# Optimization experiments

Hardware: AMD Instinct MI355X
Metric: run time of the kernel (lower is better)

Reference implementation:

```python
import jax, jax.numpy as jnp
import numpy as np

B, T, L = 16, 64, 64
DIN, D, DC, A = 512, 512, 512, 256


def setup_inputs() -> dict:
    key = jax.random.key(0)
    ks = jax.random.split(key, 16)
    g = lambda k, shape, fan: jax.random.normal(k, shape, jnp.float32) / np.float32(np.sqrt(fan))
    return {
        "X": jax.random.normal(ks[0], (B, T, DIN), jnp.float32),
        "context": jax.random.normal(ks[1], (B, L, DC), jnp.float32),
        "parent_t_seq": jax.random.randint(ks[2], (B, T), 0, T),
        "context_mask": jnp.zeros((B, L), jnp.int32),
        "mask": jnp.ones((B, T), jnp.float32),
        # fused gate weights, gate order [i, f, c, o] along last axis
        "Wx": g(ks[3], (DIN, 4 * D), DIN),
        "bx": jnp.zeros((4 * D,), jnp.float32),
        "U": g(ks[4], (D, 4 * D), D),
        "C": g(ks[5], (DC, 4 * D), DC),
        "P": g(ks[6], (D, 4 * D), D),
        "H": g(ks[7], (D, 4 * D), D),
        # context attention
        "att_ctx_W1": g(ks[8], (DC, A), DC),
        "att_b1": jnp.zeros((A,), jnp.float32),
        "att_h_W1": g(ks[9], (D, A), D),
        "att_W2": g(ks[10], (A,), A),
        "att_b2": jnp.zeros((), jnp.float32),
        # history attention
        "hatt_hist_W": g(ks[11], (D, A), D),
        "hatt_hist_b": jnp.zeros((A,), jnp.float32),
        "hatt_h_W1": g(ks[12], (D, A), D),
        "hatt_W2": g(ks[13], (A,), A),
        "hatt_b2": jnp.zeros((), jnp.float32),
    }


def reference(X, context, parent_t_seq, context_mask, mask,
              Wx, bx, U, C, P, H,
              att_ctx_W1, att_b1, att_h_W1, att_W2, att_b2,
              hatt_hist_W, hatt_hist_b, hatt_h_W1, hatt_W2, hatt_b2):
    Bb, Tt, _ = X.shape
    Dd = U.shape[0]
    x4 = X @ Wx + bx                                 # [B,T,4D] precomputed input gates
    ctx_trans = context @ att_ctx_W1 + att_b1        # [B,L,A]
    ts = jnp.arange(Tt)
    batch_idx = jnp.arange(Bb)

    def step(carry, inp):
        h, c, hist = carry                           # h,c [B,D]; hist [B,T,D]
        t, xg, m, par = inp                          # xg [B,4D], m [B], par [B]
        # --- attention over encoder context ---
        ah = jnp.tanh(ctx_trans + (h @ att_h_W1)[:, None, :])   # [B,L,A]
        raw = ah @ att_W2 + att_b2                               # [B,L]
        raw = jnp.where(context_mask > 0, -jnp.inf, raw)
        catt = jax.nn.softmax(raw, axis=-1)
        ctx_vec = jnp.einsum('bl,blc->bc', catt, context)        # [B,DC]
        # --- attention over decoding history (positions < t) ---
        hh = jnp.tanh(hist @ hatt_hist_W + hatt_hist_b + (h @ hatt_h_W1)[:, None, :])  # [B,T,A]
        hraw = hh @ hatt_W2 + hatt_b2                            # [B,T]
        hmask = (ts < t).astype(X.dtype)                         # [T]
        hexp = jnp.exp(hraw - jnp.max(hraw, axis=-1, keepdims=True)) * hmask
        hw = hexp / (jnp.sum(hexp, axis=-1, keepdims=True) + 1e-7)
        h_ctx = jnp.where(t > 0, jnp.einsum('bt,btd->bd', hw, hist), 0.0)
        # --- parent hidden state feed ---
        par_h = jnp.where(t > 0, hist[batch_idx, par], 0.0)      # [B,D]
        # --- fused LSTM gates (tree attention path: U, C, P, H terms) ---
        g = xg + h @ U + ctx_vec @ C + par_h @ P + h_ctx @ H     # [B,4D]
        gi, gf, gc, go = jnp.split(g, 4, axis=-1)
        i = jax.nn.sigmoid(gi)
        f = jax.nn.sigmoid(gf)
        o = jax.nn.sigmoid(go)
        c_new = f * c + i * jnp.tanh(gc)
        h_new = o * jnp.tanh(c_new)
        mm = m[:, None]
        h_new = (1 - mm) * h + mm * h_new
        c_new = (1 - mm) * c + mm * c_new
        hist = jax.lax.dynamic_update_slice(hist, h_new[:, None, :], (0, t, 0))
        return (h_new, c_new, hist), (h_new, c_new, ctx_vec)

    h0 = jnp.zeros((Bb, Dd), X.dtype)
    c0 = jnp.zeros((Bb, Dd), X.dtype)
    hist0 = jnp.zeros((Bb, Tt, Dd), X.dtype)
    xs = (ts, jnp.swapaxes(x4, 0, 1), mask.T, parent_t_seq.T)
    _, (hs, cs, ctxs) = jax.lax.scan(step, (h0, c0, hist0), xs)
    # back to batch-major
    return (jnp.swapaxes(hs, 0, 1), jnp.swapaxes(cs, 0, 1), jnp.swapaxes(ctxs, 0, 1))
```

## Files before the change

kernel.cpp:

```cpp
#include <hip/hip_runtime.h>
#include <cmath>
#include <cstdint>

#define NWG 256
#define NT  256

#define WS_FLAGS 0
#define WS_HC    8192
#define WS_CT    16384
#define WS_CACHE 278528
#define WS_HIST  540672
#define WS_HHP   1064960
#define WS_AHB   1196032

#define OUT_HS  0
#define OUT_CS  524288
#define OUT_CTX 1048576

#define LDS_WT   0
#define LDS_ZS   20544
#define LDS_SCR  28800
#define LDS_GLD  30848
#define LDS_ATT  30976
#define LDS_FLOATS 32448

typedef float vf4 __attribute__((ext_vector_type(4)));
typedef float vf2 __attribute__((ext_vector_type(2)));

struct CAParams {
  const float* X; const float* ctx; const int* parent; const int* cmask; const float* mask;
  const float* Wx; const float* bx; const float* U; const float* C; const float* P; const float* H;
  const float* acW1; const float* ab1; const float* ahW1; const float* aW2; const float* ab2;
  const float* hhW; const float* hhb; const float* hthW1; const float* hW2; const float* hb2;
  float* out; float* ws;
};

__device__ __forceinline__ float tanh_f(float x) {
  x = fminf(15.f, fmaxf(-15.f, x));
  float e = __expf(2.f * x);
  return (e - 1.f) / (e + 1.f);
}
__device__ __forceinline__ float sigm_f(float x) { return 1.f / (1.f + __expf(-x)); }
__device__ __forceinline__ float wsum(float v) {
  #pragma unroll
  for (int m = 32; m; m >>= 1) v += __shfl_xor(v, m, 64);
  return v;
}
__device__ __forceinline__ float wmax(float v) {
  #pragma unroll
  for (int m = 32; m; m >>= 1) v = fmaxf(v, __shfl_xor(v, m, 64));
  return v;
}
__device__ __forceinline__ float hsum32(float v) {
  #pragma unroll
  for (int m = 16; m; m >>= 1) v += __shfl_xor(v, m, 64);
  return v;
}
__device__ __forceinline__ uint32_t f2bf(float f) {
  uint32_t u = __float_as_uint(f);
  return (u + 0x7FFFu + ((u >> 16) & 1u)) >> 16;
}

__device__ __forceinline__ void bst(float* a, float v) {
  asm volatile("global_store_dword %0, %1, off sc0 sc1" :: "v"(a), "v"(v) : "memory");
}
__device__ __forceinline__ void bstu(uint32_t* a, uint32_t v) {
  asm volatile("global_store_dword %0, %1, off sc0 sc1" :: "v"(a), "v"(v) : "memory");
}
__device__ __forceinline__ void bst4(float* a, vf4 v) {
  asm volatile("global_store_dwordx4 %0, %1, off sc0 sc1" :: "v"(a), "v"(v) : "memory");
}
__device__ __forceinline__ void bld8_issue(vf4* r, const float* q0, const float* q1, const float* q2, const float* q3,
                                           const float* q4, const float* q5, const float* q6, const float* q7) {
  asm volatile(
    "global_load_dwordx4 %0, %8, off sc0 sc1\n"
    "global_load_dwordx4 %1, %9, off sc0 sc1\n"
    "global_load_dwordx4 %2, %10, off sc0 sc1\n"
    "global_load_dwordx4 %3, %11, off sc0 sc1\n"
    "global_load_dwordx4 %4, %12, off sc0 sc1\n"
    "global_load_dwordx4 %5, %13, off sc0 sc1\n"
    "global_load_dwordx4 %6, %14, off sc0 sc1\n"
    "global_load_dwordx4 %7, %15, off sc0 sc1"
    : "=&v"(r[0]),"=&v"(r[1]),"=&v"(r[2]),"=&v"(r[3]),"=&v"(r[4]),"=&v"(r[5]),"=&v"(r[6]),"=&v"(r[7])
    : "v"(q0),"v"(q1),"v"(q2),"v"(q3),"v"(q4),"v"(q5),"v"(q6),"v"(q7)
    : "memory");
}
__device__ __forceinline__ void bwait8(vf4* r) {
  asm volatile("s_waitcnt vmcnt(0)"
    : "+v"(r[0]),"+v"(r[1]),"+v"(r[2]),"+v"(r[3]),"+v"(r[4]),"+v"(r[5]),"+v"(r[6]),"+v"(r[7])
    :: "memory");
}

__global__ void __launch_bounds__(NT, 1) condatt_kernel(CAParams p) {
  extern __shared__ float lds[];
  float* wt   = lds + LDS_WT;
  float* zs   = lds + LDS_ZS;
  float* scr  = lds + LDS_SCR;
  float* gld  = lds + LDS_GLD;
  float* aw   = lds + LDS_ATT;
  float* av2  = lds + LDS_ATT + 256;
  float* abv  = lds + LDS_ATT + 512;
  float* araw = lds + LDS_ATT + 768;
  float* asmx = lds + LDS_ATT + 832;
  float* arawZ= lds + LDS_ATT + 896;
  float* hst  = lds + LDS_ATT + 960;

  const int tid = threadIdx.x;
  const int wg  = blockIdx.x;
  float* wsp = p.ws;
  unsigned* flags = (unsigned*)wsp;
  unsigned nbar = 0;

  const int base = 2 * ((wg & 7) * 32 + (wg >> 3));

  __threadfence_system();

  const int kh = tid >> 4, sub = tid & 15, bg = sub >> 2, cp = sub & 3;
  float acc[4][2] = {{0.f,0.f},{0.f,0.f},{0.f,0.f},{0.f,0.f}};
  float hprev = 0.f, cprev = 0.f;

  auto gsync = [&]() {
    asm volatile("s_waitcnt vmcnt(0)" ::: "memory");
    __syncthreads();
    ++nbar;
    if (tid == 0)
      __hip_atomic_store(&flags[wg * 16], nbar, __ATOMIC_RELAXED, __HIP_MEMORY_SCOPE_SYSTEM);
    while (__hip_atomic_load(&flags[tid * 16], __ATOMIC_RELAXED, __HIP_MEMORY_SCOPE_SYSTEM) < nbar)
      __builtin_amdgcn_s_sleep(1);
    __syncthreads();
  };

  {
    for (int j = 0; j < 4; ++j) {
      int rid = wg * 4 + j;
      __syncthreads();
      for (int i = tid; i < 512; i += NT) scr[i] = p.ctx[rid * 512 + i];
      __syncthreads();
      float a0 = 0.f, a1 = 0.f, a2 = 0.f, a3 = 0.f;
      for (int c = 0; c < 512; c += 4) {
        a0 += scr[c+0] * p.acW1[(c+0) * 256 + tid];
        a1 += scr[c+1] * p.acW1[(c+1) * 256 + tid];
        a2 += scr[c+2] * p.acW1[(c+2) * 256 + tid];
        a3 += scr[c+3] * p.acW1[(c+3) * 256 + tid];
      }
      bst(wsp + WS_CT + rid * 256 + tid, p.ab1[tid] + ((a0 + a1) + (a2 + a3)));
    }
    __syncthreads();
    const float* mats[5] = {p.Wx, p.U, p.P, p.C, p.H};
    for (int q = 0; q < 4; ++q) {
      for (int r = tid; r < 2560; r += NT) {
        int m = r >> 9, rr = r & 511;
        vf2 v = *(const vf2*)(mats[m] + rr * 2048 + base + 512 * q);
        *(vf2*)(wt + q * 5136 + r * 2) = v;
      }
    }
    {
      uint32_t* hpd = (uint32_t*)(wsp + WS_HHP);
      for (int i = wg * NT + tid; i < 131072; i += NWG * NT) {
        uint32_t lo = f2bf(p.hthW1[i]);
        uint32_t hi = f2bf(p.hhW[i]);
        bstu(hpd + i, lo | (hi << 16));
      }
      uint32_t* ahd = (uint32_t*)(wsp + WS_AHB);
      for (int j = wg * NT + tid; j < 65536; j += NWG * NT) {
        uint32_t lo = f2bf(p.ahW1[j * 2]);
        uint32_t hi = f2bf(p.ahW1[j * 2 + 1]);
        bstu(ahd + j, lo | (hi << 16));
      }
    }
    if (wg < 16)            { av2[tid] = p.aW2[tid]; }
    else if (wg < 32)       { av2[tid] = p.hW2[tid]; abv[tid] = p.hhb[tid]; }
    #pragma unroll
    for (int j = 0; j < 8; ++j) {
      int i4 = tid + j * NT, b = i4 >> 7, k0 = (i4 << 2) & 511;
      vf4 v = *(const vf4*)(p.X + (b * 64 + 0) * 512 + k0);
      *(vf4*)(zs + b * 516 + k0) = v;
    }
    __syncthreads();
  }

  auto gemm = [&](int comp) {
    const float* wp = wt + cp * 5136 + comp * 1024;
    const float* zb = zs + (bg * 4) * 516;
    #pragma unroll 4
    for (int j = 0; j < 32; ++j) {
      int k = kh + (j << 4);
      vf2 w = *(const vf2*)(wp + k * 2);
      float z0 = zb[k], z1 = zb[516 + k], z2 = zb[1032 + k], z3 = zb[1548 + k];
      acc[0][0] += z0 * w.x; acc[0][1] += z0 * w.y;
      acc[1][0] += z1 * w.x; acc[1][1] += z1 * w.y;
      acc[2][0] += z2 * w.x; acc[2][1] += z2 * w.y;
      acc[3][0] += z3 * w.x; acc[3][1] += z3 * w.y;
    }
  };

  gemm(0);
  gsync();

  for (int t = 0; t < 64; ++t) {
    if (wg < 32) {
      const int b = wg & 15;
      if (tid < 128) {
        vf4 v = {0.f, 0.f, 0.f, 0.f};
        if (t > 0) v = *(const vf4*)(wsp + WS_HIST + (b * 64 + (t - 1)) * 512 + tid * 4);
        *(vf4*)(hst + tid * 4) = v;
      }
      __syncthreads();
      if (wg < 16) {
        const uint16_t* ahb = (const uint16_t*)(wsp + WS_AHB);
        float s = 0.f;
        #pragma unroll 8
        for (int k = 0; k < 512; ++k)
          s += hst[k] * __uint_as_float((uint32_t)ahb[k * 256 + tid] << 16);
        aw[tid] = s;
        __syncthreads();
        {
          int w = tid >> 6, s32 = tid & 31, hi = (tid >> 5) & 1;
          float b2 = *p.ab2;
          for (int l = w * 2 + hi; l < 64; l += 8) {
            float sc = 0.f;
            #pragma unroll
            for (int q = 0; q < 8; ++q) { int a = s32 + (q << 5); sc += av2[a] * tanh_f(wsp[WS_CT + (b * 64 + l) * 256 + a] + aw[a]); }
            sc = hsum32(sc) + b2;
            if (s32 == 0) araw[l] = (p.cmask[b * 64 + l] > 0) ? -INFINITY : sc;
          }
        }
        __syncthreads();
        if (tid < 64) {
          float r = araw[tid];
          float mx = wmax(r);
          float e = __expf(r - mx);
          float sm = wsum(e);
          asmx[tid] = e / sm;
        }
        __syncthreads();
        {
          int db = tid & 127, half = tid >> 7;
          vf4 a0 = {0.f, 0.f, 0.f, 0.f};
          #pragma unroll 4
          for (int l = half; l < 64; l += 2) {
            float ca = asmx[l];
            vf4 cv = *(const vf4*)(p.ctx + (b * 64 + l) * 512 + db * 4);
            a0.x += ca * cv.x; a0.y += ca * cv.y; a0.z += ca * cv.z; a0.w += ca * cv.w;
          }
          *(vf4*)(scr + tid * 4) = a0;
        }
        __syncthreads();
        if (tid < 128) {
          vf4 u = *(vf4*)(scr + tid * 4), v = *(vf4*)(scr + (tid + 128) * 4);
          u.x += v.x; u.y += v.y; u.z += v.z; u.w += v.w;
          bst4(p.out + OUT_CTX + (b * 64 + t) * 512 + tid * 4, u);
        }
      } else {
        const uint32_t* hp = (const uint32_t*)(wsp + WS_HHP);
        float s1 = 0.f, s2 = 0.f;
        #pragma unroll 8
        for (int k = 0; k < 512; ++k) {
          uint32_t pk = hp[k * 256 + tid];
          float hv = hst[k];
          s1 += hv * __uint_as_float(pk << 16);
          s2 += hv * __uint_as_float(pk & 0xFFFF0000u);
        }
        aw[tid] = s1;
        if (t > 0) wsp[WS_CACHE + (b * 64 + (t - 1)) * 256 + tid] = s2;
        __syncthreads();
        {
          int w = tid >> 6, s32 = tid & 31, hi = (tid >> 5) & 1;
          float b2 = *p.hb2;
          for (int l = w * 2 + hi; l < t; l += 8) {
            float sc = 0.f;
            #pragma unroll
            for (int q = 0; q < 8; ++q) { int a = s32 + (q << 5); sc += av2[a] * tanh_f(wsp[WS_CACHE + (b * 64 + l) * 256 + a] + abv[a] + aw[a]); }
            sc = hsum32(sc) + b2;
            if (s32 == 0) araw[l] = sc;
          }
          if (tid < 32) {
            float sc = 0.f;
            #pragma unroll
            for (int q = 0; q < 8; ++q) { int a = tid + (q << 5); sc += av2[a] * tanh_f(abv[a] + aw[a]); }
            sc = hsum32(sc) + b2;
            if (tid == 0) arawZ[0] = sc;
          }
        }
        __syncthreads();
        if (tid < 64) {
          float r = (tid < t) ? araw[tid] : arawZ[0];
          float mx = wmax(r);
          float e = (tid < t) ? __expf(r - mx) : 0.f;
          float sm = wsum(e);
          asmx[tid] = e / (sm + 1e-7f);
        }
        __syncthreads();
        {
          int db = tid & 127, half = tid >> 7;
          vf4 a0 = {0.f, 0.f, 0.f, 0.f};
          #pragma unroll 4
          for (int l = half; l < t; l += 2) {
            float hv = asmx[l];
            vf4 hvv = *(const vf4*)(wsp + WS_HIST + (b * 64 + l) * 512 + db * 4);
            a0.x += hv * hvv.x; a0.y += hv * hvv.y; a0.z += hv * hvv.z; a0.w += hv * hvv.w;
          }
          *(vf4*)(scr + tid * 4) = a0;
        }
        __syncthreads();
        if (tid < 128) {
          vf4 u = *(vf4*)(scr + tid * 4), v = *(vf4*)(scr + (tid + 128) * 4);
          u.x += v.x; u.y += v.y; u.z += v.z; u.w += v.w;
          bst4(wsp + WS_HC + b * 512 + tid * 4, u);
        }
      }
    }
    __syncthreads();
    if (t == 0) {
      vf4 z = {0.f, 0.f, 0.f, 0.f};
      #pragma unroll
      for (int j = 0; j < 8; ++j) {
        int i4 = tid + j * NT, b = i4 >> 7, k0 = (i4 << 2) & 511;
        *(vf4*)(zs + b * 516 + k0) = z;
      }
    } else {
      #pragma unroll
      for (int j = 0; j < 8; ++j) {
        int i4 = tid + j * NT, b = i4 >> 7, k0 = (i4 << 2) & 511;
        vf4 v = *(const vf4*)(wsp + WS_HIST + (b * 64 + (t - 1)) * 512 + k0);
        *(vf4*)(zs + b * 516 + k0) = v;
      }
    }
    __syncthreads();
    gemm(1);
    __syncthreads();
    {
      #pragma unroll
      for (int j = 0; j < 8; ++j) {
        int i4 = tid + j * NT, b = i4 >> 7, k0 = (i4 << 2) & 511;
        int par = p.parent[b * 64 + t];
        vf4 v = {0.f, 0.f, 0.f, 0.f};
        if (t > 0 && par < t) v = *(const vf4*)(wsp + WS_HIST + (b * 64 + par) * 512 + k0);
        *(vf4*)(zs + b * 516 + k0) = v;
      }
    }
    __syncthreads();
    gemm(2);
    gsync();

    {
      #pragma unroll
      for (int j = 0; j < 8; ++j) {
        int i4 = tid + j * NT, b = i4 >> 7, k0 = (i4 << 2) & 511;
        vf4 v = *(const vf4*)(p.out + OUT_CTX + (b * 64 + t) * 512 + k0);
        *(vf4*)(zs + b * 516 + k0) = v;
      }
    }
    __syncthreads();
    vf4 rhc[8];
    {
      const float* q[8];
      #pragma unroll
      for (int j = 0; j < 8; ++j) { int i4 = tid + j * NT; q[j] = wsp + WS_HC + (i4 >> 7) * 512 + ((i4 << 2) & 511); }
      bld8_issue(rhc, q[0], q[1], q[2], q[3], q[4], q[5], q[6], q[7]);
    }
    gemm(3);
    __syncthreads();
    bwait8(rhc);
    #pragma unroll
    for (int j = 0; j < 8; ++j) { int i4 = tid + j * NT; *(vf4*)(zs + (i4 >> 7) * 516 + ((i4 << 2) & 511)) = rhc[j]; }
    __syncthreads();
    gemm(4);
    {
      float* s8 = scr + (kh * 16 + sub) * 8;
      #pragma unroll
      for (int i = 0; i < 4; ++i) { s8[i*2] = acc[i][0]; s8[i*2+1] = acc[i][1]; acc[i][0] = 0.f; acc[i][1] = 0.f; }
    }
    __syncthreads();
    if (t < 63) {
      #pragma unroll
      for (int j = 0; j < 8; ++j) {
        int i4 = tid + j * NT, b = i4 >> 7, k0 = (i4 << 2) & 511;
        vf4 v = *(const vf4*)(p.X + (b * 64 + (t + 1)) * 512 + k0);
        *(vf4*)(zs + b * 516 + k0) = v;
      }
    }
    if (tid < 128) {
      int b = tid >> 3, c = tid & 7;
      int n = base + (c & 1) + 512 * (c >> 1);
      float g = p.bx[n];
      int sidx = (b >> 2) * 4 + (c >> 1);
      int aidx = (b & 3) * 2 + (c & 1);
      #pragma unroll
      for (int k2 = 0; k2 < 16; ++k2) g += scr[(k2 * 16 + sidx) * 8 + aidx];
      gld[b * 8 + c] = g;
    }
    __syncthreads();
    if (tid < 32) {
      int b = tid >> 1, dj = tid & 1;
      int d = base + dj;
      float gi = gld[b*8 + 0 + dj];
      float gf = gld[b*8 + 2 + dj];
      float gg = gld[b*8 + 4 + dj];
      float go = gld[b*8 + 6 + dj];
      float i_ = sigm_f(gi), f_ = sigm_f(gf), o_ = sigm_f(go);
      float cn = f_ * cprev + i_ * tanh_f(gg);
      float hn = o_ * tanh_f(cn);
      float m_ = p.mask[b * 64 + t];
      hn = (1.f - m_) * hprev + m_ * hn;
      cn = (1.f - m_) * cprev + m_ * cn;
      hprev = hn; cprev = cn;
      bst(wsp + WS_HIST + (b * 64 + t) * 512 + d, hn);
      p.out[OUT_HS + (b * 64 + t) * 512 + d] = hn;
      p.out[OUT_CS + (b * 64 + t) * 512 + d] = cn;
    }
    if (t < 63) {
      gemm(0);
      gsync();
    }
  }
}

extern "C" void kernel_launch(void* const* d_in, const int* in_sizes, int n_in,
                              void* d_out, int out_size, void* d_ws, size_t ws_size,
                              hipStream_t stream) {
  CAParams p;
  p.X      = (const float*)d_in[0];
  p.ctx    = (const float*)d_in[1];
  p.parent = (const int*)  d_in[2];
  p.cmask  = (const int*)  d_in[3];
  p.mask   = (const float*)d_in[4];
  p.Wx = (const float*)d_in[5];  p.bx = (const float*)d_in[6];
  p.U  = (const float*)d_in[7];  p.C  = (const float*)d_in[8];
  p.P  = (const float*)d_in[9];  p.H  = (const float*)d_in[10];
  p.acW1 = (const float*)d_in[11]; p.ab1 = (const float*)d_in[12];
  p.ahW1 = (const float*)d_in[13]; p.aW2 = (const float*)d_in[14]; p.ab2 = (const float*)d_in[15];
  p.hhW  = (const float*)d_in[16]; p.hhb = (const float*)d_in[17];
  p.hthW1= (const float*)d_in[18]; p.hW2 = (const float*)d_in[19]; p.hb2 = (const float*)d_in[20];
  p.out = (float*)d_out;
  p.ws  = (float*)d_ws;

  (void)hipMemsetAsync(d_ws, 0, 16384, stream);

  static_assert(LDS_FLOATS * 4 <= 160 * 1024, "LDS budget");
  (void)hipFuncSetAttribute((const void*)condatt_kernel,
                      hipFuncAttributeMaxDynamicSharedMemorySize, LDS_FLOATS * 4);
  hipLaunchKernelGGL(condatt_kernel, dim3(NWG), dim3(NT), LDS_FLOATS * 4, stream, p);
}
```

Measured before the change: 2.165 ms.

## Split per-step attention across 128 workgroups with flag-synced partial score exchange

Per-batch context and history attention now runs on 128 workgroups instead of 32. Each group of four workgroups handles one slice of the attention dimension, computes partial scores, and exchanges them through a workspace buffer guarded by per-workgroup flags. The score reduction, softmax and weighted sum are moved after the gate GEMMs, so the attention partials overlap with gemm(1) and gemm(2) rather than running serially before them. The aim is to shorten the serial attention critical path each timestep, at the cost of extra global traffic, point-to-point spin waits and a redundant softmax in every workgroup of a group.

```diff
diff --git a/kernel.cpp b/kernel.cpp
--- a/kernel.cpp
+++ b/kernel.cpp
@@ -6,12 +6,13 @@
 #define NT  256
 
 #define WS_FLAGS 0
-#define WS_HC    8192
-#define WS_CT    16384
-#define WS_CACHE 278528
-#define WS_HIST  540672
-#define WS_HHP   1064960
-#define WS_AHB   1196032
+#define WS_PSC   4096
+#define WS_HC    20480
+#define WS_CT    28672
+#define WS_CACHE 290816
+#define WS_HIST  552960
+#define WS_HHP   1077248
+#define WS_AHB   1208320
 
 #define OUT_HS  0
 #define OUT_CS  524288
@@ -22,7 +23,7 @@
 #define LDS_SCR  28800
 #define LDS_GLD  30848
 #define LDS_ATT  30976
-#define LDS_FLOATS 32448
+#define LDS_FLOATS 31904
 
 typedef float vf4 __attribute__((ext_vector_type(4)));
 typedef float vf2 __attribute__((ext_vector_type(2)));
@@ -69,6 +70,18 @@
 }
 __device__ __forceinline__ void bst4(float* a, vf4 v) {
   asm volatile("global_store_dwordx4 %0, %1, off sc0 sc1" :: "v"(a), "v"(v) : "memory");
+}
+__device__ __forceinline__ vf4 bld4s(const float* a0, const float* a1, const float* a2, const float* a3) {
+  float r0, r1, r2, r3;
+  asm volatile(
+    "global_load_dword %0, %4, off sc0 sc1\n"
+    "global_load_dword %1, %5, off sc0 sc1\n"
+    "global_load_dword %2, %6, off sc0 sc1\n"
+    "global_load_dword %3, %7, off sc0 sc1\n"
+    "s_waitcnt vmcnt(0)"
+    : "=&v"(r0),"=&v"(r1),"=&v"(r2),"=&v"(r3)
+    : "v"(a0),"v"(a1),"v"(a2),"v"(a3) : "memory");
+  vf4 v; v.x = r0; v.y = r1; v.z = r2; v.w = r3; return v;
 }
 __device__ __forceinline__ void bld8_issue(vf4* r, const float* q0, const float* q1, const float* q2, const float* q3,
                                            const float* q4, const float* q5, const float* q6, const float* q7) {
@@ -101,9 +114,7 @@
   float* av2  = lds + LDS_ATT + 256;
   float* abv  = lds + LDS_ATT + 512;
   float* araw = lds + LDS_ATT + 768;
-  float* asmx = lds + LDS_ATT + 832;
-  float* arawZ= lds + LDS_ATT + 896;
-  float* hst  = lds + LDS_ATT + 960;
+  float* asmx = lds + LDS_ATT + 864;
 
   const int tid = threadIdx.x;
   const int wg  = blockIdx.x;
@@ -112,6 +123,12 @@
   unsigned nbar = 0;
 
   const int base = 2 * ((wg & 7) * 32 + (wg >> 3));
+
+  const bool isAtt  = wg < 128;
+  const bool isHist = wg >= 64;
+  const int  ab   = (wg & 63) >> 2;
+  const int  Q    = wg & 3;
+  const int  grp0 = (wg & 64) + ab * 4;
 
   __threadfence_system();
 
@@ -168,8 +185,10 @@
         bstu(ahd + j, lo | (hi << 16));
       }
     }
-    if (wg < 16)            { av2[tid] = p.aW2[tid]; }
-    else if (wg < 32)       { av2[tid] = p.hW2[tid]; abv[tid] = p.hhb[tid]; }
+    if (isAtt) {
+      if (!isHist) { av2[tid] = p.aW2[tid]; }
+      else         { av2[tid] = p.hW2[tid]; abv[tid] = p.hhb[tid]; }
+    }
     #pragma unroll
     for (int j = 0; j < 8; ++j) {
       int i4 = tid + j * NT, b = i4 >> 7, k0 = (i4 << 2) & 511;
@@ -194,139 +213,127 @@
     }
   };
 
+  const float ab2f = *p.ab2;
+  const float hb2f = *p.hb2;
+
   gemm(0);
   gsync();
 
   for (int t = 0; t < 64; ++t) {
-    if (wg < 32) {
-      const int b = wg & 15;
-      if (tid < 128) {
-        vf4 v = {0.f, 0.f, 0.f, 0.f};
-        if (t > 0) v = *(const vf4*)(wsp + WS_HIST + (b * 64 + (t - 1)) * 512 + tid * 4);
-        *(vf4*)(hst + tid * 4) = v;
-      }
-      __syncthreads();
-      if (wg < 16) {
-        const uint16_t* ahb = (const uint16_t*)(wsp + WS_AHB);
-        float s = 0.f;
-        #pragma unroll 8
-        for (int k = 0; k < 512; ++k)
-          s += hst[k] * __uint_as_float((uint32_t)ahb[k * 256 + tid] << 16);
-        aw[tid] = s;
+    __syncthreads();
+    if (t == 0) {
+      vf4 z = {0.f, 0.f, 0.f, 0.f};
+      #pragma unroll
+      for (int j = 0; j < 8; ++j) {
+        int i4 = tid + j * NT, b = i4 >> 7, k0 = (i4 << 2) & 511;
+        *(vf4*)(zs + b * 516 + k0) = z;
+      }
+    } else {
+      #pragma unroll
+      for (int j = 0; j < 8; ++j) {
+        int i4 = tid + j * NT, b = i4 >> 7, k0 = (i4 << 2) & 511;
+        vf4 v = *(const vf4*)(wsp + WS_HIST + (b * 64 + (t - 1)) * 512 + k0);
+        *(vf4*)(zs + b * 516 + k0) = v;
+      }
+    }
+    __syncthreads();
+
+    if (isAtt) {
+      const float* hb = zs + ab * 516;
+      if (!isHist) {
+        const uint32_t* ahd = (const uint32_t*)(wsp + WS_AHB);
+        int pl = tid & 31, kq = tid >> 5;
+        int pcolI = Q * 32 + pl;
+        float s0 = 0.f, s1 = 0.f;
+        #pragma unroll 16
+        for (int i = 0; i < 64; ++i) {
+          int k = kq * 64 + i;
+          uint32_t pk = ahd[k * 128 + pcolI];
+          float hv = hb[k];
+          s0 += hv * __uint_as_float(pk << 16);
+          s1 += hv * __uint_as_float(pk & 0xFFFF0000u);
+        }
+        scr[(kq * 32 + pl) * 2 + 0] = s0;
+        scr[(kq * 32 + pl) * 2 + 1] = s1;
+        __syncthreads();
+        if (tid < 64) {
+          float s = 0.f;
+          #pragma unroll
+          for (int k8 = 0; k8 < 8; ++k8) s += scr[(k8 * 32 + (tid >> 1)) * 2 + (tid & 1)];
+          aw[tid] = s;
+        }
         __syncthreads();
         {
           int w = tid >> 6, s32 = tid & 31, hi = (tid >> 5) & 1;
-          float b2 = *p.ab2;
           for (int l = w * 2 + hi; l < 64; l += 8) {
             float sc = 0.f;
             #pragma unroll
-            for (int q = 0; q < 8; ++q) { int a = s32 + (q << 5); sc += av2[a] * tanh_f(wsp[WS_CT + (b * 64 + l) * 256 + a] + aw[a]); }
-            sc = hsum32(sc) + b2;
-            if (s32 == 0) araw[l] = (p.cmask[b * 64 + l] > 0) ? -INFINITY : sc;
+            for (int q = 0; q < 2; ++q) {
+              int al = s32 + (q << 5), ag = Q * 64 + al;
+              sc += av2[ag] * tanh_f(wsp[WS_CT + (ab * 64 + l) * 256 + ag] + aw[al]);
+            }
+            sc = hsum32(sc);
+            if (s32 == 0) araw[l] = sc;
           }
         }
+        __syncthreads();
+        if (tid < 16) bst4(wsp + WS_PSC + wg * 128 + tid * 4, *(vf4*)(araw + tid * 4));
+      } else {
+        const uint32_t* hpd = (const uint32_t*)(wsp + WS_HHP);
+        int al = tid & 63, kq = tid >> 6;
+        float s1 = 0.f, s2 = 0.f;
+        #pragma unroll 16
+        for (int i = 0; i < 128; ++i) {
+          int k = kq * 128 + i;
+          uint32_t pk = hpd[k * 256 + Q * 64 + al];
+          float hv = hb[k];
+          s1 += hv * __uint_as_float(pk << 16);
+          s2 += hv * __uint_as_float(pk & 0xFFFF0000u);
+        }
+        scr[kq * 64 + al] = s1;
+        scr[256 + kq * 64 + al] = s2;
         __syncthreads();
         if (tid < 64) {
-          float r = araw[tid];
-          float mx = wmax(r);
-          float e = __expf(r - mx);
-          float sm = wsum(e);
-          asmx[tid] = e / sm;
-        }
-        __syncthreads();
-        {
-          int db = tid & 127, half = tid >> 7;
-          vf4 a0 = {0.f, 0.f, 0.f, 0.f};
-          #pragma unroll 4
-          for (int l = half; l < 64; l += 2) {
-            float ca = asmx[l];
-            vf4 cv = *(const vf4*)(p.ctx + (b * 64 + l) * 512 + db * 4);
-            a0.x += ca * cv.x; a0.y += ca * cv.y; a0.z += ca * cv.z; a0.w += ca * cv.w;
-          }
-          *(vf4*)(scr + tid * 4) = a0;
-        }
-        __syncthreads();
-        if (tid < 128) {
-          vf4 u = *(vf4*)(scr + tid * 4), v = *(vf4*)(scr + (tid + 128) * 4);
-          u.x += v.x; u.y += v.y; u.z += v.z; u.w += v.w;
-          bst4(p.out + OUT_CTX + (b * 64 + t) * 512 + tid * 4, u);
-        }
-      } else {
-        const uint32_t* hp = (const uint32_t*)(wsp + WS_HHP);
-        float s1 = 0.f, s2 = 0.f;
-        #pragma unroll 8
-        for (int k = 0; k < 512; ++k) {
-          uint32_t pk = hp[k * 256 + tid];
-          float hv = hst[k];
-          s1 += hv * __uint_as_float(pk << 16);
-          s2 += hv * __uint_as_float(pk & 0xFFFF0000u);
-        }
-        aw[tid] = s1;
-        if (t > 0) wsp[WS_CACHE + (b * 64 + (t - 1)) * 256 + tid] = s2;
+          float sa = 0.f, sb = 0.f;
+          #pragma unroll
+          for (int k4 = 0; k4 < 4; ++k4) { sa += scr[k4 * 64 + tid]; sb += scr[256 + k4 * 64 + tid]; }
+          aw[tid] = sa;
+          if (t > 0) wsp[WS_CACHE + (ab * 64 + (t - 1)) * 256 + Q * 64 + tid] = sb;
+        }
         __syncthreads();
         {
           int w = tid >> 6, s32 = tid & 31, hi = (tid >> 5) & 1;
-          float b2 = *p.hb2;
           for (int l = w * 2 + hi; l < t; l += 8) {
             float sc = 0.f;
             #pragma unroll
-            for (int q = 0; q < 8; ++q) { int a = s32 + (q << 5); sc += av2[a] * tanh_f(wsp[WS_CACHE + (b * 64 + l) * 256 + a] + abv[a] + aw[a]); }
-            sc = hsum32(sc) + b2;
+            for (int q = 0; q < 2; ++q) {
+              int al2 = s32 + (q << 5), ag = Q * 64 + al2;
+              sc += av2[ag] * tanh_f(wsp[WS_CACHE + (ab * 64 + l) * 256 + ag] + abv[ag] + aw[al2]);
+            }
+            sc = hsum32(sc);
             if (s32 == 0) araw[l] = sc;
           }
           if (tid < 32) {
             float sc = 0.f;
             #pragma unroll
-            for (int q = 0; q < 8; ++q) { int a = tid + (q << 5); sc += av2[a] * tanh_f(abv[a] + aw[a]); }
-            sc = hsum32(sc) + b2;
-            if (tid == 0) arawZ[0] = sc;
+            for (int q = 0; q < 2; ++q) {
+              int al2 = tid + (q << 5), ag = Q * 64 + al2;
+              sc += av2[ag] * tanh_f(abv[ag] + aw[al2]);
+            }
+            sc = hsum32(sc);
+            if (tid == 0) araw[64] = sc;
           }
         }
         __syncthreads();
-        if (tid < 64) {
-          float r = (tid < t) ? araw[tid] : arawZ[0];
-          float mx = wmax(r);
-          float e = (tid < t) ? __expf(r - mx) : 0.f;
-          float sm = wsum(e);
-          asmx[tid] = e / (sm + 1e-7f);
-        }
-        __syncthreads();
-        {
-          int db = tid & 127, half = tid >> 7;
-          vf4 a0 = {0.f, 0.f, 0.f, 0.f};
-          #pragma unroll 4
-          for (int l = half; l < t; l += 2) {
-            float hv = asmx[l];
-            vf4 hvv = *(const vf4*)(wsp + WS_HIST + (b * 64 + l) * 512 + db * 4);
-            a0.x += hv * hvv.x; a0.y += hv * hvv.y; a0.z += hv * hvv.z; a0.w += hv * hvv.w;
-          }
-          *(vf4*)(scr + tid * 4) = a0;
-        }
-        __syncthreads();
-        if (tid < 128) {
-          vf4 u = *(vf4*)(scr + tid * 4), v = *(vf4*)(scr + (tid + 128) * 4);
-          u.x += v.x; u.y += v.y; u.z += v.z; u.w += v.w;
-          bst4(wsp + WS_HC + b * 512 + tid * 4, u);
-        }
-      }
-    }
-    __syncthreads();
-    if (t == 0) {
-      vf4 z = {0.f, 0.f, 0.f, 0.f};
-      #pragma unroll
-      for (int j = 0; j < 8; ++j) {
-        int i4 = tid + j * NT, b = i4 >> 7, k0 = (i4 << 2) & 511;
-        *(vf4*)(zs + b * 516 + k0) = z;
-      }
-    } else {
-      #pragma unroll
-      for (int j = 0; j < 8; ++j) {
-        int i4 = tid + j * NT, b = i4 >> 7, k0 = (i4 << 2) & 511;
-        vf4 v = *(const vf4*)(wsp + WS_HIST + (b * 64 + (t - 1)) * 512 + k0);
-        *(vf4*)(zs + b * 516 + k0) = v;
-      }
-    }
-    __syncthreads();
+        if (tid < 16) bst4(wsp + WS_PSC + wg * 128 + tid * 4, *(vf4*)(araw + tid * 4));
+        if (tid == 16) bst(wsp + WS_PSC + wg * 128 + 64, araw[64]);
+      }
+      asm volatile("s_waitcnt vmcnt(0)" ::: "memory");
+      __syncthreads();
+      if (tid == 0)
+        __hip_atomic_store(&flags[wg * 16 + 2], (unsigned)(t + 1), __ATOMIC_RELAXED, __HIP_MEMORY_SCOPE_SYSTEM);
+    }
+
     gemm(1);
     __syncthreads();
     {
@@ -341,6 +348,65 @@
     }
     __syncthreads();
     gemm(2);
+
+    if (isAtt) {
+      if (tid < 4)
+        while (__hip_atomic_load(&flags[(grp0 + tid) * 16 + 2], __ATOMIC_RELAXED, __HIP_MEMORY_SCOPE_SYSTEM) < (unsigned)(t + 1))
+          __builtin_amdgcn_s_sleep(1);
+      __syncthreads();
+      const int NL = isHist ? 65 : 64;
+      if (tid < NL) {
+        const float* b0 = wsp + WS_PSC + grp0 * 128 + tid;
+        vf4 s4 = bld4s(b0, b0 + 128, b0 + 256, b0 + 384);
+        float s = ((s4.x + s4.y) + s4.z) + s4.w;
+        if (!isHist) araw[tid] = (p.cmask[ab * 64 + tid] > 0) ? -INFINITY : (s + ab2f);
+        else         araw[tid] = s + hb2f;
+      }
+      __syncthreads();
+      if (tid < 64) {
+        if (!isHist) {
+          float r = araw[tid];
+          float mx = wmax(r), e = __expf(r - mx), sm = wsum(e);
+          asmx[tid] = e / sm;
+        } else {
+          float r = (tid < t) ? araw[tid] : araw[64];
+          float mx = wmax(r);
+          float e = (tid < t) ? __expf(r - mx) : 0.f;
+          float sm = wsum(e);
+          asmx[tid] = e / (sm + 1e-7f);
+        }
+      }
+      __syncthreads();
+      {
+        int dv = tid & 31, lq = tid >> 5;
+        vf4 a0 = {0.f, 0.f, 0.f, 0.f};
+        if (!isHist) {
+          for (int l = lq; l < 64; l += 8) {
+            float ca = asmx[l];
+            vf4 cv = *(const vf4*)(p.ctx + (ab * 64 + l) * 512 + Q * 128 + dv * 4);
+            a0.x += ca * cv.x; a0.y += ca * cv.y; a0.z += ca * cv.z; a0.w += ca * cv.w;
+          }
+        } else {
+          for (int l = lq; l < t; l += 8) {
+            float hv = asmx[l];
+            vf4 cv = *(const vf4*)(wsp + WS_HIST + (ab * 64 + l) * 512 + Q * 128 + dv * 4);
+            a0.x += hv * cv.x; a0.y += hv * cv.y; a0.z += hv * cv.z; a0.w += hv * cv.w;
+          }
+        }
+        *(vf4*)(scr + tid * 4) = a0;
+      }
+      __syncthreads();
+      if (tid < 32) {
+        vf4 u = {0.f, 0.f, 0.f, 0.f};
+        #pragma unroll
+        for (int j = 0; j < 8; ++j) {
+          vf4 v = *(vf4*)(scr + (j * 32 + tid) * 4);
+          u.x += v.x; u.y += v.y; u.z += v.z; u.w += v.w;
+        }
+        if (!isHist) bst4(p.out + OUT_CTX + (ab * 64 + t) * 512 + Q * 128 + tid * 4, u);
+        else         bst4(wsp + WS_HC + ab * 512 + Q * 128 + tid * 4, u);
+      }
+    }
     gsync();
 
     {
```

Measured after the change: 2.628 ms. 21.4% more time.

## Transpose bf16 attention weights to column-major and keep U/C weights in registers

Applied to the files above, without the earlier changes.

The packed bf16 attention projection weights are now stored column-major, so each thread reads its own column with 128-bit vector loads instead of strided scalar loads. The U and C weight slices are preloaded into registers once, so the two per-step GEMMs that use them no longer read weights from LDS. The LDS weight stride is padded slightly. This cuts memory traffic on the serial recurrent path but adds about 128 VGPRs of live register state, which could lower occupancy or cause spills. The per-thread column reads are no longer coalesced across a wave.

```diff
diff --git a/kernel.cpp b/kernel.cpp
--- a/kernel.cpp
+++ b/kernel.cpp
@@ -18,14 +18,15 @@
 #define OUT_CTX 1048576
 
 #define LDS_WT   0
-#define LDS_ZS   20544
-#define LDS_SCR  28800
-#define LDS_GLD  30848
-#define LDS_ATT  30976
-#define LDS_FLOATS 32448
+#define LDS_ZS   20560
+#define LDS_SCR  28816
+#define LDS_GLD  30864
+#define LDS_ATT  30992
+#define LDS_FLOATS 32464
 
 typedef float vf4 __attribute__((ext_vector_type(4)));
 typedef float vf2 __attribute__((ext_vector_type(2)));
+typedef uint32_t vu4 __attribute__((ext_vector_type(4)));
 
 struct CAParams {
   const float* X; const float* ctx; const int* parent; const int* cmask; const float* mask;
@@ -60,6 +61,8 @@
   uint32_t u = __float_as_uint(f);
   return (u + 0x7FFFu + ((u >> 16) & 1u)) >> 16;
 }
+__device__ __forceinline__ float bflo(uint32_t pk) { return __uint_as_float(pk << 16); }
+__device__ __forceinline__ float bfhi(uint32_t pk) { return __uint_as_float(pk & 0xFFFF0000u); }
 
 __device__ __forceinline__ void bst(float* a, float v) {
   asm volatile("global_store_dword %0, %1, off sc0 sc1" :: "v"(a), "v"(v) : "memory");
@@ -151,21 +154,23 @@
       for (int r = tid; r < 2560; r += NT) {
         int m = r >> 9, rr = r & 511;
         vf2 v = *(const vf2*)(mats[m] + rr * 2048 + base + 512 * q);
-        *(vf2*)(wt + q * 5136 + r * 2) = v;
+        *(vf2*)(wt + q * 5140 + r * 2) = v;
       }
     }
     {
       uint32_t* hpd = (uint32_t*)(wsp + WS_HHP);
-      for (int i = wg * NT + tid; i < 131072; i += NWG * NT) {
-        uint32_t lo = f2bf(p.hthW1[i]);
-        uint32_t hi = f2bf(p.hhW[i]);
-        bstu(hpd + i, lo | (hi << 16));
+      for (int idx = wg * NT + tid; idx < 131072; idx += NWG * NT) {
+        int col = idx & 255, k = idx >> 8;
+        uint32_t lo = f2bf(p.hthW1[k * 256 + col]);
+        uint32_t hi = f2bf(p.hhW[k * 256 + col]);
+        bstu(hpd + col * 512 + k, lo | (hi << 16));
       }
       uint32_t* ahd = (uint32_t*)(wsp + WS_AHB);
-      for (int j = wg * NT + tid; j < 65536; j += NWG * NT) {
-        uint32_t lo = f2bf(p.ahW1[j * 2]);
-        uint32_t hi = f2bf(p.ahW1[j * 2 + 1]);
-        bstu(ahd + j, lo | (hi << 16));
+      for (int idx = wg * NT + tid; idx < 65536; idx += NWG * NT) {
+        int col = idx & 255, kk = idx >> 8;
+        uint32_t lo = f2bf(p.ahW1[(2 * kk) * 256 + col]);
+        uint32_t hi = f2bf(p.ahW1[(2 * kk + 1) * 256 + col]);
+        bstu(ahd + col * 256 + kk, lo | (hi << 16));
       }
     }
     if (wg < 16)            { av2[tid] = p.aW2[tid]; }
@@ -179,8 +184,16 @@
     __syncthreads();
   }
 
+  vf2 wU[32], wC[32];
+  #pragma unroll
+  for (int j = 0; j < 32; ++j) {
+    int k = kh + (j << 4);
+    wU[j] = *(const vf2*)(wt + cp * 5140 + 1 * 1024 + k * 2);
+    wC[j] = *(const vf2*)(wt + cp * 5140 + 3 * 1024 + k * 2);
+  }
+
   auto gemm = [&](int comp) {
-    const float* wp = wt + cp * 5136 + comp * 1024;
+    const float* wp = wt + cp * 5140 + comp * 1024;
     const float* zb = zs + (bg * 4) * 516;
     #pragma unroll 4
     for (int j = 0; j < 32; ++j) {
@@ -193,6 +206,19 @@
       acc[3][0] += z3 * w.x; acc[3][1] += z3 * w.y;
     }
   };
+  auto gemmR = [&](const vf2* wr) {
+    const float* zb = zs + (bg * 4) * 516;
+    #pragma unroll
+    for (int j = 0; j < 32; ++j) {
+      int k = kh + (j << 4);
+      vf2 w = wr[j];
+      float z0 = zb[k], z1 = zb[516 + k], z2 = zb[1032 + k], z3 = zb[1548 + k];
+      acc[0][0] += z0 * w.x; acc[0][1] += z0 * w.y;
+      acc[1][0] += z1 * w.x; acc[1][1] += z1 * w.y;
+      acc[2][0] += z2 * w.x; acc[2][1] += z2 * w.y;
+      acc[3][0] += z3 * w.x; acc[3][1] += z3 * w.y;
+    }
+  };
 
   gemm(0);
   gsync();
@@ -207,11 +233,17 @@
       }
       __syncthreads();
       if (wg < 16) {
-        const uint16_t* ahb = (const uint16_t*)(wsp + WS_AHB);
+        const vu4* acol = (const vu4*)((const uint32_t*)(wsp + WS_AHB) + tid * 256);
         float s = 0.f;
         #pragma unroll 8
-        for (int k = 0; k < 512; ++k)
-          s += hst[k] * __uint_as_float((uint32_t)ahb[k * 256 + tid] << 16);
+        for (int i = 0; i < 64; ++i) {
+          vu4 pk = acol[i];
+          int k0 = i * 8;
+          s += hst[k0+0] * bflo(pk.x) + hst[k0+1] * bfhi(pk.x)
+             + hst[k0+2] * bflo(pk.y) + hst[k0+3] * bfhi(pk.y)
+             + hst[k0+4] * bflo(pk.z) + hst[k0+5] * bfhi(pk.z)
+             + hst[k0+6] * bflo(pk.w) + hst[k0+7] * bfhi(pk.w);
+        }
         aw[tid] = s;
         __syncthreads();
         {
@@ -252,14 +284,15 @@
           bst4(p.out + OUT_CTX + (b * 64 + t) * 512 + tid * 4, u);
         }
       } else {
-        const uint32_t* hp = (const uint32_t*)(wsp + WS_HHP);
+        const vu4* wcol = (const vu4*)((const uint32_t*)(wsp + WS_HHP) + tid * 512);
         float s1 = 0.f, s2 = 0.f;
         #pragma unroll 8
-        for (int k = 0; k < 512; ++k) {
-          uint32_t pk = hp[k * 256 + tid];
-          float hv = hst[k];
-          s1 += hv * __uint_as_float(pk << 16);
-          s2 += hv * __uint_as_float(pk & 0xFFFF0000u);
+        for (int i = 0; i < 128; ++i) {
+          vu4 pk = wcol[i];
+          int k0 = i * 4;
+          float h0 = hst[k0+0], h1 = hst[k0+1], h2 = hst[k0+2], h3 = hst[k0+3];
+          s1 += h0 * bflo(pk.x) + h1 * bflo(pk.y) + h2 * bflo(pk.z) + h3 * bflo(pk.w);
+          s2 += h0 * bfhi(pk.x) + h1 * bfhi(pk.y) + h2 * bfhi(pk.z) + h3 * bfhi(pk.w);
         }
         aw[tid] = s1;
         if (t > 0) wsp[WS_CACHE + (b * 64 + (t - 1)) * 256 + tid] = s2;
@@ -327,7 +360,7 @@
       }
     }
     __syncthreads();
-    gemm(1);
+    gemmR(wU);
     __syncthreads();
     {
       #pragma unroll
@@ -359,7 +392,7 @@
       for (int j = 0; j < 8; ++j) { int i4 = tid + j * NT; q[j] = wsp + WS_HC + (i4 >> 7) * 512 + ((i4 << 2) & 511); }
       bld8_issue(rhc, q[0], q[1], q[2], q[3], q[4], q[5], q[6], q[7]);
     }
-    gemm(3);
+    gemmR(wC);
     __syncthreads();
     bwait8(rhc);
     #pragma unroll
```

Result: slower. 3.121 ms (+44.2%).
